# Kernel tuning notes

Hardware: AMD Instinct MI355X
Metric: run time of the kernel (lower is better)

The kernel has to match this reference:

```python
import jax, jax.numpy as jnp
import numpy as np

N, D, M, L, DEPTH, WIDTH, MPTS = 2048, 64, 2048, 16, 3, 128, 64
WIN = 2 * L + 1  # 33


def setup_inputs() -> dict:
    key = jax.random.key(0)
    ks = jax.random.split(key, 6)
    # xavier-normal-ish scales to keep sigmoids in a reasonable range
    s0 = float(np.sqrt(2.0 / (D + WIDTH)))
    s1 = float(np.sqrt(2.0 / (2 * WIDTH)))
    s2 = float(np.sqrt(2.0 / (WIDTH + WIN)))
    return {
        "u": jax.random.normal(ks[0], (MPTS, D), dtype=jnp.float32),
        "weight0": jax.random.normal(ks[1], (WIN, WIDTH, D), dtype=jnp.float32) * s0,
        "bias0": jnp.zeros((WIN, WIDTH, 1), dtype=jnp.float32),
        "weight": jax.random.normal(ks[2], (DEPTH - 1, WIN, WIDTH, WIDTH), dtype=jnp.float32) * s1,
        "bias": jnp.zeros((DEPTH - 1, WIN, WIDTH, 1), dtype=jnp.float32),
        "weight_final": jax.random.normal(ks[3], (M, WIN, WIDTH), dtype=jnp.float32) * s2,
        "bias_final": jnp.zeros((M, WIN, 1), dtype=jnp.float32),
        "xi": jax.random.normal(ks[4], (M, N + 2 * L), dtype=jnp.float32) * 0.1,
    }


def reference(u, weight0, bias0, weight, bias, weight_final, bias_final, xi):
    sig = jax.nn.sigmoid
    # first_step: shared per-frequency MLP stack
    u1 = sig(jnp.einsum('jkl,ml->jkm', weight0, u) + bias0)
    for i in range(weight.shape[0]):  # depth-1 hidden layers (small fixed count)
        u1 = sig(jnp.einsum('jkl,jlm->jkm', weight[i], u1) + bias[i])
    G = sig(jnp.einsum('ijk,jkm->ijm', weight_final, u1) + bias_final)
    # sliding-window weighted sum over spectral coeffs, vectorized as a 1D
    # cross-correlation: out[n, p] = sum_{m,j} xi[m, n+j] * G[m, j, p]
    kernel = jnp.transpose(G, (2, 0, 1))
    out = jax.lax.conv_general_dilated(
        xi[None],  # [1, M, N+2L]
        kernel,
        window_strides=(1,),
        padding='VALID',
        dimension_numbers=('NCH', 'OIH', 'NCH'),
    )  # [1, MPTS, N]
    return out[0].T  # [N, MPTS] == torch.cat over iter_prod
```

## Files before the change

kernel.cpp:

```cpp
#include <hip/hip_runtime.h>

#define WIN 33
#define WIDTH 128
#define MPTS 64
#define NN 2048
#define MM 2048
#define DD 64
#define NQ 2080

typedef __bf16 bf16x8 __attribute__((ext_vector_type(8)));
typedef float f32x4 __attribute__((ext_vector_type(4)));

__device__ __forceinline__ unsigned short f2bf(float x) {
  union { float f; unsigned int u; } v; v.f = x;
  unsigned int r = v.u + 0x7FFFu + ((v.u >> 16) & 1u);
  return (unsigned short)(r >> 16);
}
__device__ __forceinline__ float sigf(float x) { return 1.0f / (1.0f + __expf(-x)); }

__global__ __launch_bounds__(256) void k_transpose(const float* __restrict__ xi,
                                                   unsigned short* __restrict__ xiT) {
  __shared__ float ts[64 * 37];
  int qb = blockIdx.x * 32;
  int mb = blockIdx.y * 64;
#pragma unroll
  for (int c = threadIdx.x; c < 512; c += 256) {
    int row = c >> 3, c8 = c & 7;
    float4 v = *(const float4*)&xi[(size_t)(mb + row) * NQ + qb + (c8 << 2)];
    ts[row * 37 + (c8 << 2) + 0] = v.x;
    ts[row * 37 + (c8 << 2) + 1] = v.y;
    ts[row * 37 + (c8 << 2) + 2] = v.z;
    ts[row * 37 + (c8 << 2) + 3] = v.w;
  }
  __syncthreads();
#pragma unroll
  for (int c = threadIdx.x; c < 512; c += 256) {
    int r = c >> 4, mq = c & 15;
    ushort4 h;
    h.x = f2bf(ts[(mq * 4 + 0) * 37 + r]);
    h.y = f2bf(ts[(mq * 4 + 1) * 37 + r]);
    h.z = f2bf(ts[(mq * 4 + 2) * 37 + r]);
    h.w = f2bf(ts[(mq * 4 + 3) * 37 + r]);
    *(ushort4*)&xiT[(size_t)(qb + r) * MM + mb + (mq << 2)] = h;
  }
}

__global__ __launch_bounds__(256) void k_mlp(const float* __restrict__ u,
                                             const float* __restrict__ w0,
                                             const float* __restrict__ b0,
                                             const float* __restrict__ w,
                                             const float* __restrict__ bias,
                                             unsigned short* __restrict__ u1bf) {
  constexpr int WS = 72;
  constexpr int AS = 136;
  __shared__ unsigned short ws[128 * WS];
  __shared__ unsigned short actA[64 * AS];
  __shared__ unsigned short actB[64 * AS];
  __shared__ float biass[128];
  int j = blockIdx.x;
  int tid = threadIdx.x;
  int wv = tid >> 6, lane = tid & 63, l15 = lane & 15, l4 = lane >> 4;

#pragma unroll
  for (int c = tid; c < 1024; c += 256) {
    int p = c >> 4, d4 = (c & 15) << 2;
    float4 v = *(const float4*)&u[(size_t)p * DD + d4];
    ushort4 h; h.x = f2bf(v.x); h.y = f2bf(v.y); h.z = f2bf(v.z); h.w = f2bf(v.w);
    *(ushort4*)&actA[p * AS + d4] = h;
  }
#pragma unroll
  for (int c = tid; c < 2048; c += 256) {
    int k = c >> 4, d4 = (c & 15) << 2;
    float4 v = *(const float4*)&w0[((size_t)j * 128 + k) * DD + d4];
    ushort4 h; h.x = f2bf(v.x); h.y = f2bf(v.y); h.z = f2bf(v.z); h.w = f2bf(v.w);
    *(ushort4*)&ws[k * WS + d4] = h;
  }
  if (tid < 128) biass[tid] = b0[j * 128 + tid];
  __syncthreads();

  {
    f32x4 acc[2][4] = {};
#pragma unroll
    for (int t = 0; t < 2; ++t) {
      int col = (t << 5) + (l4 << 3);
      bf16x8 a[2], b[4];
#pragma unroll
      for (int s = 0; s < 2; ++s)
        a[s] = *(const bf16x8*)&ws[(wv * 32 + s * 16 + l15) * WS + col];
#pragma unroll
      for (int q = 0; q < 4; ++q)
        b[q] = *(const bf16x8*)&actA[(q * 16 + l15) * AS + col];
#pragma unroll
      for (int s = 0; s < 2; ++s)
#pragma unroll
        for (int q = 0; q < 4; ++q)
          acc[s][q] = __builtin_amdgcn_mfma_f32_16x16x32_bf16(a[s], b[q], acc[s][q], 0, 0, 0);
    }
#pragma unroll
    for (int s = 0; s < 2; ++s)
#pragma unroll
      for (int q = 0; q < 4; ++q) {
        int p = q * 16 + l15;
#pragma unroll
        for (int r = 0; r < 4; ++r) {
          int k = wv * 32 + s * 16 + (l4 << 2) + r;
          actB[p * AS + k] = f2bf(sigf(acc[s][q][r] + biass[k]));
        }
      }
  }

  unsigned short* ain = actB;
  unsigned short* aout = actA;
#pragma unroll
  for (int i = 0; i < 2; ++i) {
    f32x4 acc[2][4] = {};
    const float* wbase = w + ((size_t)i * WIN + j) * 128 * 128;
#pragma unroll
    for (int h = 0; h < 2; ++h) {
      __syncthreads();
#pragma unroll
      for (int c = tid; c < 2048; c += 256) {
        int k = c >> 4, d4 = (c & 15) << 2;
        float4 v = *(const float4*)&wbase[(size_t)k * 128 + h * 64 + d4];
        ushort4 hh; hh.x = f2bf(v.x); hh.y = f2bf(v.y); hh.z = f2bf(v.z); hh.w = f2bf(v.w);
        *(ushort4*)&ws[k * WS + d4] = hh;
      }
      if (h == 0 && tid < 128) biass[tid] = bias[((size_t)i * WIN + j) * 128 + tid];
      __syncthreads();
#pragma unroll
      for (int t = 0; t < 2; ++t) {
        int col = (t << 5) + (l4 << 3);
        bf16x8 a[2], b[4];
#pragma unroll
        for (int s = 0; s < 2; ++s)
          a[s] = *(const bf16x8*)&ws[(wv * 32 + s * 16 + l15) * WS + col];
#pragma unroll
        for (int q = 0; q < 4; ++q)
          b[q] = *(const bf16x8*)&ain[(q * 16 + l15) * AS + h * 64 + col];
#pragma unroll
        for (int s = 0; s < 2; ++s)
#pragma unroll
          for (int q = 0; q < 4; ++q)
            acc[s][q] = __builtin_amdgcn_mfma_f32_16x16x32_bf16(a[s], b[q], acc[s][q], 0, 0, 0);
      }
    }
#pragma unroll
    for (int s = 0; s < 2; ++s)
#pragma unroll
      for (int q = 0; q < 4; ++q) {
        int p = q * 16 + l15;
#pragma unroll
        for (int r = 0; r < 4; ++r) {
          int k = wv * 32 + s * 16 + (l4 << 2) + r;
          aout[p * AS + k] = f2bf(sigf(acc[s][q][r] + biass[k]));
        }
      }
    unsigned short* t2 = ain; ain = aout; aout = t2;
  }
  __syncthreads();
#pragma unroll
  for (int c = tid; c < 1024; c += 256) {
    int p = c >> 4, k8 = (c & 15) << 3;
    uint4 v = *(const uint4*)&ain[p * AS + k8];
    *(uint4*)&u1bf[((size_t)j * MPTS + p) * WIDTH + k8] = v;
  }
}

__global__ __launch_bounds__(256) void k_final(const float* __restrict__ wf,
                                               const float* __restrict__ bfin,
                                               const unsigned short* __restrict__ u1bf,
                                               unsigned short* __restrict__ Gt2) {
  constexpr int KP = 136;
  __shared__ unsigned short As[64 * KP];
  __shared__ unsigned short Bs[64 * KP];
  int bid = blockIdx.x;
  int j = bid >> 5;
  int m0 = (bid & 31) << 6;
#pragma unroll
  for (int c = threadIdx.x; c < 64 * 32; c += 256) {
    int row = c >> 5, f4 = c & 31;
    float4 v = *(const float4*)(wf + ((size_t)(m0 + row) * WIN + j) * WIDTH + (f4 << 2));
    ushort4 h;
    h.x = f2bf(v.x); h.y = f2bf(v.y); h.z = f2bf(v.z); h.w = f2bf(v.w);
    *(ushort4*)(&As[row * KP + (f4 << 2)]) = h;
  }
#pragma unroll
  for (int c = threadIdx.x; c < 64 * 16; c += 256) {
    int p = c >> 4, ch = c & 15;
    uint4 v = *(const uint4*)(u1bf + (size_t)(j * MPTS + p) * WIDTH + (ch << 3));
    *(uint4*)(&Bs[p * KP + (ch << 3)]) = v;
  }
  __syncthreads();
  int wv = threadIdx.x >> 6, lane = threadIdx.x & 63;
  int l15 = lane & 15, l4 = lane >> 4;
  f32x4 acc[4] = {};
#pragma unroll
  for (int t = 0; t < 4; ++t) {
    int col = (t << 5) + (l4 << 3);
    bf16x8 a = *(const bf16x8*)(&As[(wv * 16 + l15) * KP + col]);
#pragma unroll
    for (int q = 0; q < 4; ++q) {
      bf16x8 bb = *(const bf16x8*)(&Bs[(q * 16 + l15) * KP + col]);
      acc[q] = __builtin_amdgcn_mfma_f32_16x16x32_bf16(a, bb, acc[q], 0, 0, 0);
    }
  }
#pragma unroll
  for (int q = 0; q < 4; ++q) {
    int mr = m0 + wv * 16 + (l4 << 2);
    int p = q * 16 + l15;
    float z0 = acc[q][0] + bfin[(size_t)(mr + 0) * WIN + j];
    float z1 = acc[q][1] + bfin[(size_t)(mr + 1) * WIN + j];
    float z2 = acc[q][2] + bfin[(size_t)(mr + 2) * WIN + j];
    float z3 = acc[q][3] + bfin[(size_t)(mr + 3) * WIN + j];
    ushort4 st;
    st.x = f2bf(sigf(z0)); st.y = f2bf(sigf(z1));
    st.z = f2bf(sigf(z2)); st.w = f2bf(sigf(z3));
    *(ushort4*)(&Gt2[(size_t)(j * MPTS + p) * MM + mr]) = st;
  }
}

__global__ __launch_bounds__(256) void k_conv(const unsigned short* __restrict__ xiT,
                                              const unsigned short* __restrict__ Gt2,
                                              float* __restrict__ out) {
  extern __shared__ unsigned short lds[];
  unsigned short* As = lds;
  unsigned short* Bs = lds + 160 * 40;
  int bid = blockIdx.x;
  int n0 = (bid & 15) << 7;
  int mp = bid >> 4;
  int tid = threadIdx.x;
  int wv = tid >> 6, lane = tid & 63, l15 = lane & 15, l4 = lane >> 4;
  f32x4 acc[2][4] = {};
#pragma unroll
  for (int half = 0; half < 2; ++half) {
    int m0 = (mp << 6) + (half << 5);
    __syncthreads();
    for (int c = tid; c < 640; c += 256) {
      int row = c >> 2, g = c & 3;
      uint4 v = *(const uint4*)(xiT + (size_t)(n0 + row) * MM + m0 + (g << 3));
      *(uint4*)(&As[row * 40 + (g << 3)]) = v;
    }
    for (int ph = 0; ph < 3; ++ph) {
      int jb = ph * 11;
      if (ph) __syncthreads();
      for (int c = tid; c < 2816; c += 256) {
        int jp = c >> 2, g = c & 3;
        uint4 v = *(const uint4*)(Gt2 + ((size_t)(jb << 6) + jp) * MM + m0 + (g << 3));
        *(uint4*)(&Bs[jp * 40 + (g << 3)]) = v;
      }
      __syncthreads();
      bf16x8 a[2], b[4];
#pragma unroll
      for (int s = 0; s < 2; ++s)
        a[s] = *(const bf16x8*)(&As[(wv * 32 + s * 16 + l15 + jb) * 40 + (l4 << 3)]);
#pragma unroll
      for (int q = 0; q < 4; ++q)
        b[q] = *(const bf16x8*)(&Bs[(q * 16 + l15) * 40 + (l4 << 3)]);
#pragma unroll
      for (int jj = 0; jj < 11; ++jj) {
        bf16x8 an[2], bn[4];
        if (jj < 10) {
#pragma unroll
          for (int s = 0; s < 2; ++s)
            an[s] = *(const bf16x8*)(&As[(wv * 32 + s * 16 + l15 + jb + jj + 1) * 40 + (l4 << 3)]);
#pragma unroll
          for (int q = 0; q < 4; ++q)
            bn[q] = *(const bf16x8*)(&Bs[((jj + 1) * 64 + q * 16 + l15) * 40 + (l4 << 3)]);
        }
#pragma unroll
        for (int s = 0; s < 2; ++s)
#pragma unroll
          for (int q = 0; q < 4; ++q)
            acc[s][q] = __builtin_amdgcn_mfma_f32_16x16x32_bf16(a[s], b[q], acc[s][q], 0, 0, 0);
#pragma unroll
        for (int s = 0; s < 2; ++s) a[s] = an[s];
#pragma unroll
        for (int q = 0; q < 4; ++q) b[q] = bn[q];
      }
    }
  }
#pragma unroll
  for (int s = 0; s < 2; ++s)
#pragma unroll
    for (int q = 0; q < 4; ++q) {
      int nr = n0 + wv * 32 + s * 16 + (l4 << 2);
      int p = q * 16 + l15;
#pragma unroll
      for (int i = 0; i < 4; ++i)
        atomicAdd(&out[(size_t)(nr + i) * MPTS + p], acc[s][q][i]);
    }
}

extern "C" void kernel_launch(void* const* d_in, const int* in_sizes, int n_in,
                              void* d_out, int out_size, void* d_ws, size_t ws_size,
                              hipStream_t stream) {
  const float* u    = (const float*)d_in[0];
  const float* w0   = (const float*)d_in[1];
  const float* b0   = (const float*)d_in[2];
  const float* w    = (const float*)d_in[3];
  const float* bias = (const float*)d_in[4];
  const float* wf   = (const float*)d_in[5];
  const float* bfin = (const float*)d_in[6];
  const float* xi   = (const float*)d_in[7];
  float* out = (float*)d_out;
  char* ws = (char*)d_ws;
  unsigned short* xiT  = (unsigned short*)(ws);
  unsigned short* Gt2  = (unsigned short*)(ws + 8519680);
  unsigned short* u1bf = (unsigned short*)(ws + 17170432);

  hipFuncSetAttribute(reinterpret_cast<const void*>(&k_conv),
                      hipFuncAttributeMaxDynamicSharedMemorySize, 69120);

  hipMemsetAsync(out, 0, (size_t)out_size * sizeof(float), stream);
  k_transpose<<<dim3(65, 32), 256, 0, stream>>>(xi, xiT);
  k_mlp<<<WIN, 256, 0, stream>>>(u, w0, b0, w, bias, u1bf);
  k_final<<<33 * 32, 256, 0, stream>>>(wf, bfin, u1bf, Gt2);
  k_conv<<<512, 256, 69120, stream>>>(xiT, Gt2, out);
}
```

Before: 180.4 us.

## Load conv tiles directly into LDS with global_load_lds and XOR-swizzled layout

Replaces the register-staged global-to-LDS copies in the conv kernel with direct global_load_lds 16-byte transfers. The A tile now holds the full 64-column m range in one XOR-swizzled buffer loaded once instead of per half, and B is stored in an instruction-ordered layout that matches the MFMA read pattern. Block-to-tile mapping is also swapped so consecutive blocks share the same n rows, and LDS use shrinks slightly. The intent is to cut VGPR traffic, load instructions and bank conflicts, but it relies on the correctness of swizzle and slot index math.

```diff
diff --git a/kernel.cpp b/kernel.cpp
--- a/kernel.cpp
+++ b/kernel.cpp
@@ -17,6 +17,12 @@
   return (unsigned short)(r >> 16);
 }
 __device__ __forceinline__ float sigf(float x) { return 1.0f / (1.0f + __expf(-x)); }
+
+__device__ __forceinline__ void gll16(const unsigned short* g, unsigned short* l) {
+  __builtin_amdgcn_global_load_lds(
+      (const __attribute__((address_space(1))) unsigned int*)g,
+      (__attribute__((address_space(3))) unsigned int*)l, 16, 0, 0);
+}
 
 __global__ __launch_bounds__(256) void k_transpose(const float* __restrict__ xi,
                                                    unsigned short* __restrict__ xiT) {
@@ -224,48 +230,67 @@
                                               float* __restrict__ out) {
   extern __shared__ unsigned short lds[];
   unsigned short* As = lds;
-  unsigned short* Bs = lds + 160 * 40;
+  unsigned short* Bs = lds + 10240;
   int bid = blockIdx.x;
-  int n0 = (bid & 15) << 7;
-  int mp = bid >> 4;
+  int mp = bid & 31;
+  int n0 = (bid >> 5) << 7;
+  int m0 = mp << 6;
   int tid = threadIdx.x;
   int wv = tid >> 6, lane = tid & 63, l15 = lane & 15, l4 = lane >> 4;
+
+#pragma unroll
+  for (int k = 0; k < 5; ++k) {
+    int instr = wv * 5 + k;
+    int s = (instr << 6) + lane;
+    int row = s >> 3;
+    int c = (s & 7) ^ (row & 7);
+    gll16(xiT + (size_t)(n0 + row) * MM + m0 + (c << 3), As + (instr << 9));
+  }
+
   f32x4 acc[2][4] = {};
 #pragma unroll
   for (int half = 0; half < 2; ++half) {
-    int m0 = (mp << 6) + (half << 5);
-    __syncthreads();
-    for (int c = tid; c < 640; c += 256) {
-      int row = c >> 2, g = c & 3;
-      uint4 v = *(const uint4*)(xiT + (size_t)(n0 + row) * MM + m0 + (g << 3));
-      *(uint4*)(&As[row * 40 + (g << 3)]) = v;
-    }
+    int mh = m0 + (half << 5);
+    int h4 = half << 2;
+#pragma unroll
     for (int ph = 0; ph < 3; ++ph) {
       int jb = ph * 11;
-      if (ph) __syncthreads();
-      for (int c = tid; c < 2816; c += 256) {
-        int jp = c >> 2, g = c & 3;
-        uint4 v = *(const uint4*)(Gt2 + ((size_t)(jb << 6) + jp) * MM + m0 + (g << 3));
-        *(uint4*)(&Bs[jp * 40 + (g << 3)]) = v;
+      if (half | ph) __syncthreads();
+#pragma unroll
+      for (int k = 0; k < 11; ++k) {
+        int instr = wv * 11 + k;
+        int s = (instr << 6) + lane;
+        int jj = s >> 8, g = (s >> 6) & 3, p = s & 63;
+        gll16(Gt2 + ((size_t)((jb + jj) << 6) + p) * MM + mh + (g << 3),
+              Bs + (instr << 9));
       }
       __syncthreads();
+
       bf16x8 a[2], b[4];
 #pragma unroll
-      for (int s = 0; s < 2; ++s)
-        a[s] = *(const bf16x8*)(&As[(wv * 32 + s * 16 + l15 + jb) * 40 + (l4 << 3)]);
-#pragma unroll
-      for (int q = 0; q < 4; ++q)
-        b[q] = *(const bf16x8*)(&Bs[(q * 16 + l15) * 40 + (l4 << 3)]);
+      for (int s = 0; s < 2; ++s) {
+        int row = wv * 32 + s * 16 + l15 + jb;
+        a[s] = *(const bf16x8*)&As[row * 64 + (((h4 | l4) ^ (row & 7)) << 3)];
+      }
+#pragma unroll
+      for (int q = 0; q < 4; ++q) {
+        int slot = (l4 << 6) + (q << 4) + l15;
+        b[q] = *(const bf16x8*)&Bs[slot << 3];
+      }
 #pragma unroll
       for (int jj = 0; jj < 11; ++jj) {
         bf16x8 an[2], bn[4];
         if (jj < 10) {
 #pragma unroll
-          for (int s = 0; s < 2; ++s)
-            an[s] = *(const bf16x8*)(&As[(wv * 32 + s * 16 + l15 + jb + jj + 1) * 40 + (l4 << 3)]);
-#pragma unroll
-          for (int q = 0; q < 4; ++q)
-            bn[q] = *(const bf16x8*)(&Bs[((jj + 1) * 64 + q * 16 + l15) * 40 + (l4 << 3)]);
+          for (int s = 0; s < 2; ++s) {
+            int row = wv * 32 + s * 16 + l15 + jb + jj + 1;
+            an[s] = *(const bf16x8*)&As[row * 64 + (((h4 | l4) ^ (row & 7)) << 3)];
+          }
+#pragma unroll
+          for (int q = 0; q < 4; ++q) {
+            int slot = ((((jj + 1) << 2) + l4) << 6) + (q << 4) + l15;
+            bn[q] = *(const bf16x8*)&Bs[slot << 3];
+          }
         }
 #pragma unroll
         for (int s = 0; s < 2; ++s)
@@ -309,11 +334,11 @@
   unsigned short* u1bf = (unsigned short*)(ws + 17170432);
 
   hipFuncSetAttribute(reinterpret_cast<const void*>(&k_conv),
-                      hipFuncAttributeMaxDynamicSharedMemorySize, 69120);
+                      hipFuncAttributeMaxDynamicSharedMemorySize, 65536);
 
   hipMemsetAsync(out, 0, (size_t)out_size * sizeof(float), stream);
   k_transpose<<<dim3(65, 32), 256, 0, stream>>>(xi, xiT);
   k_mlp<<<WIN, 256, 0, stream>>>(u, w0, b0, w, bias, u1bf);
   k_final<<<33 * 32, 256, 0, stream>>>(wf, bfin, u1bf, Gt2);
-  k_conv<<<512, 256, 69120, stream>>>(xiT, Gt2, out);
-}
+  k_conv<<<512, 256, 65536, stream>>>(xiT, Gt2, out);
+}
```

Measured after the change: 177.4 us. About the same (-1.7%).
